# Kernel optimization log

Hardware: AMD Instinct MI355X
Metric: run time of the kernel (lower is better)

## Reference

```python
import jax, jax.numpy as jnp
import numpy as np

N = 30000      # nodes
E = 480000     # edges per relation (avg degree 16)
H = 4          # GAT heads
D = 64         # out_size per head
F1, F2 = 256, 128   # per-metapath input feature dims
SIN = 256      # sen_in_size
HD = H * D     # 256, semantic-attention in_size
OUT = 64       # final out_size


def _gat(feat, src, dst, W, al, ar, b):
    """DGL GATConv (eval mode, dropout=0), activation=relu6."""
    h = (feat @ W).reshape(N, H, D)                     # [N,H,D]
    el = (h * al).sum(-1)                               # [N,H]
    er = (h * ar).sum(-1)                               # [N,H]
    e = jax.nn.leaky_relu(el[src] + er[dst], 0.2)       # [E,H]
    m = jax.ops.segment_max(e, dst, N)                  # edge-softmax over incoming edges
    p = jnp.exp(e - m[dst])
    s = jax.ops.segment_sum(p, dst, N)
    a = p / s[dst]                                      # [E,H]
    out = jax.ops.segment_sum(a[:, :, None] * h[src], dst, N)  # [N,H,D]
    out = out + b.reshape(1, H, D)
    return jnp.clip(out, 0.0, 6.0).reshape(N, H * D)    # relu6, flatten(1)


def _gcn_layer(x, src, dst, W, b):
    """DGL GraphConv, norm='both': D_in^{-1/2} A D_out^{-1/2} X W (+ b)."""
    ones = jnp.ones(src.shape[0], x.dtype)
    deg_o = jnp.clip(jax.ops.segment_sum(ones, src, N), 1.0, None)
    deg_i = jnp.clip(jax.ops.segment_sum(ones, dst, N), 1.0, None)
    h = (x @ W) * (deg_o[:, None] ** -0.5)
    h = jax.ops.segment_sum(h[src], dst, N) * (deg_i[:, None] ** -0.5)
    return h if b is None else h + b


def setup_inputs():
    key = jax.random.key(0)
    ks = jax.random.split(key, 28)
    f32 = jnp.float32
    nrm = lambda k, shp: jax.random.normal(k, shp, f32) * 0.05
    ri = lambda k, shp: jax.random.randint(k, shp, 0, N, jnp.int32)
    return dict(
        feat0=jax.random.normal(ks[0], (N, F1), f32),
        feat1=jax.random.normal(ks[1], (N, F2), f32),
        sen_feat=jax.random.normal(ks[2], (N, SIN), f32),
        Wgat0=nrm(ks[11], (F1, H * D)), al0=nrm(ks[12], (H, D)), ar0=nrm(ks[13], (H, D)), b0=nrm(ks[14], (H * D,)),
        Wgat1=nrm(ks[15], (F2, H * D)), al1=nrm(ks[16], (H, D)), ar1=nrm(ks[17], (H, D)), b1=nrm(ks[18], (H * D,)),
        Wp1=nrm(ks[19], (HD, OUT)), bp1=nrm(ks[20], (OUT,)), wp2=nrm(ks[21], (OUT,)),
        Wf=nrm(ks[22], (HD, OUT)), bf=nrm(ks[23], (OUT,)),
        Wg1=nrm(ks[24], (SIN, OUT)), bg1=nrm(ks[25], (OUT,)), Wg2=nrm(ks[26], (OUT, OUT)),
        src0=ri(ks[3], (E,)), dst0=ri(ks[4], (E,)),
        src1=ri(ks[5], (E,)), dst1=ri(ks[6], (E,)),
        gsrc=ri(ks[7], (E,)), gdst=ri(ks[8], (E,)),
        asrc=ri(ks[9], (E,)), adst=ri(ks[10], (E,)),
        k=10,
    )


def reference(feat0, feat1, sen_feat,
              Wgat0, al0, ar0, b0, Wgat1, al1, ar1, b1,
              Wp1, bp1, wp2, Wf, bf, Wg1, bg1, Wg2,
              src0, dst0, src1, dst1, gsrc, gdst, asrc, adst, k):
    # per-metapath GAT embeddings
    z0 = _gat(feat0, src0, dst0, Wgat0, al0, ar0, b0)   # [N, HD]
    z1 = _gat(feat1, src1, dst1, Wgat1, al1, ar1, b1)   # [N, HD]
    z = jnp.stack([z0, z1], axis=1)                     # [N, M=2, HD]
    # PathAttention (semantic attention over metapaths)
    w = jnp.tanh(z @ Wp1 + bp1) @ wp2                   # [N, M]
    beta = jax.nn.softmax(w.mean(0))                    # [M]
    fused = jnp.einsum('m,nmf->nf', beta, z)            # [N, HD]
    Femb = fused @ Wf + bf                              # [N, OUT]
    # two-layer GCN on the sentence graph
    p1 = jnp.tanh(_gcn_layer(sen_feat, gsrc, gdst, Wg1, bg1))
    P = _gcn_layer(p1, gsrc, gdst, Wg2, None)           # [N, OUT]
    # spectral loss: fuse embeddings, trace of Laplacian quadratic form on first k dims
    Z = 0.5 * (Femb + P)                                # [N, OUT]
    Zk = Z[:, :k]
    diff = Zk[asrc] - Zk[adst]
    tr = 0.5 * jnp.sum(diff * diff)                     # tr(Zk^T (D - A) Zk)
    return (tr, Z)
```

## Files before the change

### kernel.cpp

```cpp
#include <hip/hip_runtime.h>
#include <math.h>

#define NN 30000
#define NE 480000
#define NBLK 118
#define NMT 235
#define NTRB 1875
#define CAPD 128

typedef unsigned short ushort_t;
typedef unsigned int uint_t;
typedef __attribute__((ext_vector_type(8))) short short8;
typedef __attribute__((ext_vector_type(4))) float f32x4;

__device__ __forceinline__ ushort_t f2bf(float x) {
  uint_t u = __float_as_uint(x);
  u = (u + 0x7FFF + ((u >> 16) & 1)) >> 16;
  return (ushort_t)u;
}
__device__ __forceinline__ float bf2f(ushort_t v) {
  return __uint_as_float(((uint_t)v) << 16);
}

__device__ __forceinline__ float wred(float v) {
#pragma unroll
  for (int off = 32; off > 0; off >>= 1) v += __shfl_xor(v, off);
  return v;
}

__global__ void prep_kernel(float4* __restrict__ zp, const float* __restrict__ W0,
                            const float* __restrict__ W1, const float* __restrict__ W2,
                            const float* __restrict__ W3, const float* __restrict__ W4,
                            ushort_t* __restrict__ T0, ushort_t* __restrict__ T1,
                            ushort_t* __restrict__ T2, ushort_t* __restrict__ T3,
                            ushort_t* __restrict__ T4) {
  int id = blockIdx.x * 256 + threadIdx.x;
  if (id < 52501) {
    zp[id] = make_float4(0.f, 0.f, 0.f, 0.f);
    return;
  }
  int wid = id - 52501;
  const float* W;
  ushort_t* T;
  int K, N, base;
  if (wid < 65536) { W = W0; T = T0; K = 256; N = 256; base = 0; }
  else if (wid < 98304) { W = W1; T = T1; K = 128; N = 256; base = 65536; }
  else if (wid < 114688) { W = W2; T = T2; K = 256; N = 64; base = 98304; }
  else if (wid < 131072) { W = W3; T = T3; K = 256; N = 64; base = 114688; }
  else if (wid < 147456) { W = W4; T = T4; K = 256; N = 64; base = 131072; }
  else return;
  int l = wid - base;
  int k = l / N, n = l - k * N;
  T[(size_t)n * K + k] = f2bf(W[l]);
}


__device__ __forceinline__ void mfma_core_f32(const float* __restrict__ A0,
                                              const ushort_t* __restrict__ BT, int K, int bm,
                                              short* __restrict__ As, short* __restrict__ Bs,
                                              f32x4 acc[2][4]) {
  int tid = threadIdx.x;
  int lane = tid & 63, w = tid >> 6;
  int q = lane >> 4, mr = lane & 15;
#pragma unroll 1
  for (int k0 = 0; k0 < K; k0 += 32) {
    {
      int r = tid >> 1, hf = tid & 1;
      int gr = bm + r;
      float4 f0 = make_float4(0.f, 0.f, 0.f, 0.f), f1 = f0, f2 = f0, f3 = f0;
      if (gr < NN) {
        const float4* pa = (const float4*)(A0 + (size_t)gr * K + k0 + hf * 16);
        f0 = pa[0]; f1 = pa[1]; f2 = pa[2]; f3 = pa[3];
      }
      short8 lo, hi;
      lo[0] = (short)f2bf(f0.x); lo[1] = (short)f2bf(f0.y);
      lo[2] = (short)f2bf(f0.z); lo[3] = (short)f2bf(f0.w);
      lo[4] = (short)f2bf(f1.x); lo[5] = (short)f2bf(f1.y);
      lo[6] = (short)f2bf(f1.z); lo[7] = (short)f2bf(f1.w);
      hi[0] = (short)f2bf(f2.x); hi[1] = (short)f2bf(f2.y);
      hi[2] = (short)f2bf(f2.z); hi[3] = (short)f2bf(f2.w);
      hi[4] = (short)f2bf(f3.x); hi[5] = (short)f2bf(f3.y);
      hi[6] = (short)f2bf(f3.z); hi[7] = (short)f2bf(f3.w);
      short* dst = As + r * 40 + hf * 16;
      *(short8*)(dst) = lo;
      *(short8*)(dst + 8) = hi;
    }
    {
      int n = tid >> 2, qk = tid & 3;
      short8 bv = *(const short8*)((const short*)BT + (size_t)n * K + k0 + qk * 8);
      *(short8*)(Bs + n * 40 + qk * 8) = bv;
    }
    __syncthreads();
    short8 a0 = *(short8*)(As + (w * 32 + mr) * 40 + q * 8);
    short8 a1 = *(short8*)(As + (w * 32 + 16 + mr) * 40 + q * 8);
#pragma unroll
    for (int j = 0; j < 4; ++j) {
      short8 b = *(short8*)(Bs + (j * 16 + mr) * 40 + q * 8);
      acc[0][j] = __builtin_amdgcn_mfma_f32_16x16x32_bf16(a0, b, acc[0][j], 0, 0, 0);
      acc[1][j] = __builtin_amdgcn_mfma_f32_16x16x32_bf16(a1, b, acc[1][j], 0, 0, 0);
    }
    __syncthreads();
  }
}

__device__ __forceinline__ void mfma_core2_f32(const float* __restrict__ A0,
                                               const ushort_t* __restrict__ BT, int K, int bm,
                                               short* __restrict__ As, short* __restrict__ Bs,
                                               f32x4 acc[2][8]) {
  int tid = threadIdx.x;
  int lane = tid & 63, w = tid >> 6;
  int q = lane >> 4, mr = lane & 15;
#pragma unroll 1
  for (int k0 = 0; k0 < K; k0 += 32) {
    {
      int r = tid >> 1, hf = tid & 1;
      int gr = bm + r;
      float4 f0 = make_float4(0.f, 0.f, 0.f, 0.f), f1 = f0, f2 = f0, f3 = f0;
      if (gr < NN) {
        const float4* pa = (const float4*)(A0 + (size_t)gr * K + k0 + hf * 16);
        f0 = pa[0]; f1 = pa[1]; f2 = pa[2]; f3 = pa[3];
      }
      short8 lo, hi;
      lo[0] = (short)f2bf(f0.x); lo[1] = (short)f2bf(f0.y);
      lo[2] = (short)f2bf(f0.z); lo[3] = (short)f2bf(f0.w);
      lo[4] = (short)f2bf(f1.x); lo[5] = (short)f2bf(f1.y);
      lo[6] = (short)f2bf(f1.z); lo[7] = (short)f2bf(f1.w);
      hi[0] = (short)f2bf(f2.x); hi[1] = (short)f2bf(f2.y);
      hi[2] = (short)f2bf(f2.z); hi[3] = (short)f2bf(f2.w);
      hi[4] = (short)f2bf(f3.x); hi[5] = (short)f2bf(f3.y);
      hi[6] = (short)f2bf(f3.z); hi[7] = (short)f2bf(f3.w);
      short* dst = As + r * 40 + hf * 16;
      *(short8*)(dst) = lo;
      *(short8*)(dst + 8) = hi;
    }
    {
      int n = tid >> 1, qk = tid & 1;
      const short* src = (const short*)BT + (size_t)n * K + k0 + qk * 16;
      short8 b0 = *(const short8*)src;
      short8 b1 = *(const short8*)(src + 8);
      short* d = Bs + n * 40 + qk * 16;
      *(short8*)d = b0;
      *(short8*)(d + 8) = b1;
    }
    __syncthreads();
    short8 a0 = *(short8*)(As + (w * 32 + mr) * 40 + q * 8);
    short8 a1 = *(short8*)(As + (w * 32 + 16 + mr) * 40 + q * 8);
#pragma unroll
    for (int j = 0; j < 8; ++j) {
      short8 b = *(short8*)(Bs + (j * 16 + mr) * 40 + q * 8);
      acc[0][j] = __builtin_amdgcn_mfma_f32_16x16x32_bf16(a0, b, acc[0][j], 0, 0, 0);
      acc[1][j] = __builtin_amdgcn_mfma_f32_16x16x32_bf16(a1, b, acc[1][j], 0, 0, 0);
    }
    __syncthreads();
  }
}

__device__ __forceinline__ void mfma_core2_bf(const ushort_t* __restrict__ A0,
                                              const ushort_t* __restrict__ BT, int bm,
                                              short* __restrict__ As, short* __restrict__ Bs,
                                              f32x4 acc[2][8]) {
  int tid = threadIdx.x;
  int lane = tid & 63, w = tid >> 6;
  int q = lane >> 4, mr = lane & 15;
#pragma unroll 1
  for (int k0 = 0; k0 < 256; k0 += 32) {
    {
      int r = tid >> 1, hf = tid & 1;
      int gr = bm + r;
      short8 v0 = {0, 0, 0, 0, 0, 0, 0, 0}, v1 = v0;
      if (gr < NN) {
        const short* p0 = (const short*)A0 + (size_t)gr * 256 + k0 + hf * 16;
        v0 = *(const short8*)p0;
        v1 = *(const short8*)(p0 + 8);
      }
      short* dst = As + r * 40 + hf * 16;
      *(short8*)(dst) = v0;
      *(short8*)(dst + 8) = v1;
    }
    {
      int n = tid >> 1, qk = tid & 1;
      const short* src = (const short*)BT + (size_t)n * 256 + k0 + qk * 16;
      short8 b0 = *(const short8*)src;
      short8 b1 = *(const short8*)(src + 8);
      short* d = Bs + n * 40 + qk * 16;
      *(short8*)d = b0;
      *(short8*)(d + 8) = b1;
    }
    __syncthreads();
    short8 a0 = *(short8*)(As + (w * 32 + mr) * 40 + q * 8);
    short8 a1 = *(short8*)(As + (w * 32 + 16 + mr) * 40 + q * 8);
#pragma unroll
    for (int j = 0; j < 8; ++j) {
      short8 b = *(short8*)(Bs + (j * 16 + mr) * 40 + q * 8);
      acc[0][j] = __builtin_amdgcn_mfma_f32_16x16x32_bf16(a0, b, acc[0][j], 0, 0, 0);
      acc[1][j] = __builtin_amdgcn_mfma_f32_16x16x32_bf16(a1, b, acc[1][j], 0, 0, 0);
    }
    __syncthreads();
  }
}

__global__ __launch_bounds__(256) void mfma_all_kernel(
    const float* __restrict__ feat0, const float* __restrict__ feat1,
    const float* __restrict__ sen, const ushort_t* __restrict__ WT0,
    const ushort_t* __restrict__ WT1, const ushort_t* __restrict__ Wg1T,
    ushort_t* __restrict__ h0, ushort_t* __restrict__ h1, ushort_t* __restrict__ gcnA,
    const float* __restrict__ al0, const float* __restrict__ ar0, float* __restrict__ el0,
    float* __restrict__ er0, const float* __restrict__ al1, const float* __restrict__ ar1,
    float* __restrict__ el1, float* __restrict__ er1, const float* __restrict__ rdo) {
  __shared__ short As[128 * 40];
  __shared__ short Bs[128 * 40];
  int y = blockIdx.y;
  int bm = blockIdx.x * 128;
  int lane = threadIdx.x & 63, w = threadIdx.x >> 6;
  int q = lane >> 4, mr = lane & 15;
  if (y < 4) {
    int gsel = y >> 1, p = y & 1;
    const float* A = gsel ? feat1 : feat0;
    int K = gsel ? 128 : 256;
    const ushort_t* WT = gsel ? WT1 : WT0;
    ushort_t* H = gsel ? h1 : h0;
    const float* al = gsel ? al1 : al0;
    const float* ar = gsel ? ar1 : ar0;
    float* el = gsel ? el1 : el0;
    float* er = gsel ? er1 : er0;
    f32x4 acc[2][8];
#pragma unroll
    for (int i = 0; i < 2; ++i)
#pragma unroll
      for (int j = 0; j < 8; ++j) acc[i][j] = (f32x4){0.f, 0.f, 0.f, 0.f};
    mfma_core2_f32(A, WT + (size_t)p * 128 * K, K, bm, As, Bs, acc);
    float alv[8], arv[8];
#pragma unroll
    for (int j = 0; j < 8; ++j) {
      alv[j] = al[p * 128 + j * 16 + mr];
      arv[j] = ar[p * 128 + j * 16 + mr];
    }
#pragma unroll
    for (int i = 0; i < 2; ++i)
#pragma unroll
      for (int r = 0; r < 4; ++r) {
        int gr = bm + w * 32 + i * 16 + q * 4 + r;
        float pl0 = 0.f, pr0 = 0.f, pl1 = 0.f, pr1 = 0.f;
#pragma unroll
        for (int j = 0; j < 4; ++j) {
          pl0 = fmaf(acc[i][j][r], alv[j], pl0);
          pr0 = fmaf(acc[i][j][r], arv[j], pr0);
          pl1 = fmaf(acc[i][j + 4][r], alv[j + 4], pl1);
          pr1 = fmaf(acc[i][j + 4][r], arv[j + 4], pr1);
        }
#pragma unroll
        for (int m = 1; m < 16; m <<= 1) {
          pl0 += __shfl_xor(pl0, m);
          pr0 += __shfl_xor(pr0, m);
          pl1 += __shfl_xor(pl1, m);
          pr1 += __shfl_xor(pr1, m);
        }
        if (gr < NN) {
          if (mr == 0) {
            el[gr * 4 + 2 * p] = pl0;
            er[gr * 4 + 2 * p] = pr0;
            el[gr * 4 + 2 * p + 1] = pl1;
            er[gr * 4 + 2 * p + 1] = pr1;
          }
#pragma unroll
          for (int j = 0; j < 8; ++j)
            H[(size_t)gr * 256 + p * 128 + j * 16 + mr] = f2bf(acc[i][j][r]);
        }
      }
  } else {
    f32x4 acc[2][4];
#pragma unroll
    for (int i = 0; i < 2; ++i)
#pragma unroll
      for (int j = 0; j < 4; ++j) acc[i][j] = (f32x4){0.f, 0.f, 0.f, 0.f};
    mfma_core_f32(sen, Wg1T, 256, bm, As, Bs, acc);
#pragma unroll
    for (int i = 0; i < 2; ++i)
#pragma unroll
      for (int r = 0; r < 4; ++r) {
        int gr = bm + w * 32 + i * 16 + q * 4 + r;
        if (gr < NN) {
          float sc = rdo[gr];
#pragma unroll
          for (int j = 0; j < 4; ++j)
            gcnA[(size_t)gr * 64 + j * 16 + mr] = f2bf(acc[i][j][r] * sc);
        }
      }
  }
}

__global__ __launch_bounds__(256) void mfma_attnwf_kernel(
    const ushort_t* __restrict__ z0, const ushort_t* __restrict__ z1,
    const ushort_t* __restrict__ WpfT, const float* __restrict__ bp1,
    const float* __restrict__ wp2, float* __restrict__ pbuf, ushort_t* __restrict__ Y0,
    ushort_t* __restrict__ Y1) {
  __shared__ short As[128 * 40];
  __shared__ short Bs[128 * 40];
  __shared__ float wsum[4];
  const ushort_t* A = blockIdx.y ? z1 : z0;
  ushort_t* Y = blockIdx.y ? Y1 : Y0;
  int bm = blockIdx.x * 128;
  f32x4 acc[2][8];
#pragma unroll
  for (int i = 0; i < 2; ++i)
#pragma unroll
    for (int j = 0; j < 8; ++j) acc[i][j] = (f32x4){0.f, 0.f, 0.f, 0.f};
  mfma_core2_bf(A, WpfT, bm, As, Bs, acc);
  int lane = threadIdx.x & 63, w = threadIdx.x >> 6;
  int q = lane >> 4, mr = lane & 15;
  float local = 0.f;
#pragma unroll
  for (int j = 0; j < 4; ++j) {
    int col = j * 16 + mr;
    float bp = bp1[col], wp = wp2[col];
#pragma unroll
    for (int i = 0; i < 2; ++i)
#pragma unroll
      for (int r = 0; r < 4; ++r) {
        int gr = bm + w * 32 + i * 16 + q * 4 + r;
        if (gr < NN) local += tanhf(acc[i][j][r] + bp) * wp;
      }
  }
  local = wred(local);
  if (lane == 0) wsum[w] = local;
#pragma unroll
  for (int j = 4; j < 8; ++j) {
    int col = (j - 4) * 16 + mr;
#pragma unroll
    for (int i = 0; i < 2; ++i)
#pragma unroll
      for (int r = 0; r < 4; ++r) {
        int gr = bm + w * 32 + i * 16 + q * 4 + r;
        if (gr < NN) Y[(size_t)gr * 64 + col] = f2bf(acc[i][j][r]);
      }
  }
  __syncthreads();
  if (threadIdx.x == 0)
    pbuf[blockIdx.y * NMT + blockIdx.x] = wsum[0] + wsum[1] + wsum[2] + wsum[3];
}

__global__ void hist_kernel(const int* __restrict__ d0, const int* __restrict__ d1,
                            const int* __restrict__ d2, const int* __restrict__ d3,
                            int* __restrict__ cnt) {
  int g = blockIdx.y;
  const int* d = g == 0 ? d0 : g == 1 ? d1 : g == 2 ? d2 : d3;
  int e = blockIdx.x * 256 + threadIdx.x;
  if (e < NE) atomicAdd(&cnt[g * NN + d[e]], 1);
}

__global__ __launch_bounds__(256) void scan_blocks_kernel(const int* __restrict__ cnt,
                                                          int* __restrict__ rows,
                                                          int* __restrict__ bsum) {
  __shared__ int sm[256];
  int g = blockIdx.y, t = threadIdx.x;
  int i = blockIdx.x * 256 + t;
  int v = (i < NN) ? cnt[g * NN + i] : 0;
  sm[t] = v;
  __syncthreads();
#pragma unroll
  for (int off = 1; off < 256; off <<= 1) {
    int tmp = (t >= off) ? sm[t - off] : 0;
    __syncthreads();
    sm[t] += tmp;
    __syncthreads();
  }
  if (i < NN) rows[g * (NN + 1) + i] = sm[t] - v;
  if (t == 255) bsum[g * NBLK + blockIdx.x] = sm[255];
}

__global__ __launch_bounds__(128) void scan_tops_kernel(int* __restrict__ bsum,
                                                        int* __restrict__ boff) {
  __shared__ int sm[128];
  int g = blockIdx.y, t = threadIdx.x;
  int v = (t < NBLK) ? bsum[g * NBLK + t] : 0;
  sm[t] = v;
  __syncthreads();
#pragma unroll
  for (int off = 1; off < 128; off <<= 1) {
    int tmp = (t >= off) ? sm[t - off] : 0;
    __syncthreads();
    sm[t] += tmp;
    __syncthreads();
  }
  if (t < NBLK) boff[g * NBLK + t] = sm[t] - v;
}

__global__ void add_off_kernel(int* __restrict__ rows, const int* __restrict__ boff) {
  int g = blockIdx.y, t = threadIdx.x;
  int i = blockIdx.x * 256 + t;
  if (i < NN) rows[g * (NN + 1) + i] += boff[g * NBLK + blockIdx.x];
  if (blockIdx.x == 0 && t == 0) rows[g * (NN + 1) + NN] = NE;
}

__global__ void scatter_kernel(const int* __restrict__ s0, const int* __restrict__ s1,
                               const int* __restrict__ s2, const int* __restrict__ d0,
                               const int* __restrict__ d1, const int* __restrict__ d2,
                               const int* __restrict__ rows, int* __restrict__ cnt2,
                               int* __restrict__ cols, const int* __restrict__ cnt_deg,
                               float* __restrict__ rdo, float* __restrict__ rdi,
                               const int* __restrict__ rows_g) {
  int g = blockIdx.y;
  if (g == 3) {
    int n = blockIdx.x * 256 + threadIdx.x;
    if (n < NN) {
      rdo[n] = rsqrtf(fmaxf((float)cnt_deg[n], 1.f));
      float di = (float)(rows_g[n + 1] - rows_g[n]);
      rdi[n] = rsqrtf(fmaxf(di, 1.f));
    }
    return;
  }
  const int* sp = g == 0 ? s0 : g == 1 ? s1 : s2;
  const int* dp = g == 0 ? d0 : g == 1 ? d1 : d2;
  int e = blockIdx.x * 256 + threadIdx.x;
  if (e >= NE) return;
  int d = dp[e];
  int pos = rows[g * (NN + 1) + d] + atomicAdd(&cnt2[g * NN + d], 1);
  cols[(size_t)g * NE + pos] = sp[e];
}

__global__ __launch_bounds__(256) void gat_node_kernel(
    const int* __restrict__ rows0, const int* __restrict__ cols0, const float* __restrict__ el0,
    const float* __restrict__ er0, const ushort_t* __restrict__ h0,
    const float* __restrict__ bias0, ushort_t* __restrict__ zz0, const int* __restrict__ rows1,
    const int* __restrict__ cols1, const float* __restrict__ el1, const float* __restrict__ er1,
    const ushort_t* __restrict__ h1, const float* __restrict__ bias1,
    ushort_t* __restrict__ zz1) {
  __shared__ float aw[4][CAPD][4];
  int g = blockIdx.y;
  const int* rows = g ? rows1 : rows0;
  const int* cols = g ? cols1 : cols0;
  const float* el = g ? el1 : el0;
  const float* er = g ? er1 : er0;
  const ushort_t* h = g ? h1 : h0;
  const float* bias = g ? bias1 : bias0;
  ushort_t* z = g ? zz1 : zz0;

  int lane = threadIdx.x & 63, w = threadIdx.x >> 6;
  int n = blockIdx.x * 4 + w;
  int r0 = rows[n], r1 = rows[n + 1];
  int deg = r1 - r0;
  float4 er4 = *(const float4*)&er[n * 4];
  float s0 = 0.f, s1 = 0.f, s2 = 0.f, s3 = 0.f;
  for (int j = lane; j < deg; j += 64) {
    int s = cols[r0 + j];
    float4 elv = *(const float4*)&el[s * 4];
    float v0 = elv.x + er4.x; v0 = v0 > 0.f ? v0 : 0.2f * v0;
    float v1 = elv.y + er4.y; v1 = v1 > 0.f ? v1 : 0.2f * v1;
    float v2 = elv.z + er4.z; v2 = v2 > 0.f ? v2 : 0.2f * v2;
    float v3 = elv.w + er4.w; v3 = v3 > 0.f ? v3 : 0.2f * v3;
    float e0 = __expf(v0), e1 = __expf(v1), e2 = __expf(v2), e3 = __expf(v3);
    s0 += e0; s1 += e1; s2 += e2; s3 += e3;
    if (j < CAPD) {
      aw[w][j][0] = e0; aw[w][j][1] = e1; aw[w][j][2] = e2; aw[w][j][3] = e3;
    }
  }
  s0 = wred(s0); s1 = wred(s1); s2 = wred(s2); s3 = wred(s3);
  __syncthreads();
  int hh = lane >> 4;
  float denom = hh == 0 ? s0 : hh == 1 ? s1 : hh == 2 ? s2 : s3;
  float myer = hh == 0 ? er4.x : hh == 1 ? er4.y : hh == 2 ? er4.z : er4.w;
  float invd = (deg > 0) ? 1.f / denom : 0.f;
  float4 acc = make_float4(0.f, 0.f, 0.f, 0.f);
  int jc = deg < CAPD ? deg : CAPD;
  int j = 0;
  for (; j + 8 <= jc; j += 8) {
    int si[8];
    float ai[8];
    ushort4 ui[8];
#pragma unroll
    for (int t = 0; t < 8; ++t) {
      si[t] = cols[r0 + j + t];
      ai[t] = aw[w][j + t][hh];
    }
#pragma unroll
    for (int t = 0; t < 8; ++t) ui[t] = *(const ushort4*)&h[(size_t)si[t] * 256 + lane * 4];
#pragma unroll
    for (int t = 0; t < 8; ++t) {
      acc.x = fmaf(ai[t], bf2f(ui[t].x), acc.x);
      acc.y = fmaf(ai[t], bf2f(ui[t].y), acc.y);
      acc.z = fmaf(ai[t], bf2f(ui[t].z), acc.z);
      acc.w = fmaf(ai[t], bf2f(ui[t].w), acc.w);
    }
  }
  for (; j + 4 <= jc; j += 4) {
    int sa = cols[r0 + j], sb = cols[r0 + j + 1], sc = cols[r0 + j + 2], sd = cols[r0 + j + 3];
    float aa = aw[w][j][hh], ab = aw[w][j + 1][hh], ac = aw[w][j + 2][hh], ad = aw[w][j + 3][hh];
    ushort4 ua = *(const ushort4*)&h[(size_t)sa * 256 + lane * 4];
    ushort4 ub = *(const ushort4*)&h[(size_t)sb * 256 + lane * 4];
    ushort4 uc = *(const ushort4*)&h[(size_t)sc * 256 + lane * 4];
    ushort4 ud = *(const ushort4*)&h[(size_t)sd * 256 + lane * 4];
    acc.x = fmaf(aa, bf2f(ua.x), acc.x); acc.y = fmaf(aa, bf2f(ua.y), acc.y);
    acc.z = fmaf(aa, bf2f(ua.z), acc.z); acc.w = fmaf(aa, bf2f(ua.w), acc.w);
    acc.x = fmaf(ab, bf2f(ub.x), acc.x); acc.y = fmaf(ab, bf2f(ub.y), acc.y);
    acc.z = fmaf(ab, bf2f(ub.z), acc.z); acc.w = fmaf(ab, bf2f(ub.w), acc.w);
    acc.x = fmaf(ac, bf2f(uc.x), acc.x); acc.y = fmaf(ac, bf2f(uc.y), acc.y);
    acc.z = fmaf(ac, bf2f(uc.z), acc.z); acc.w = fmaf(ac, bf2f(uc.w), acc.w);
    acc.x = fmaf(ad, bf2f(ud.x), acc.x); acc.y = fmaf(ad, bf2f(ud.y), acc.y);
    acc.z = fmaf(ad, bf2f(ud.z), acc.z); acc.w = fmaf(ad, bf2f(ud.w), acc.w);
  }
  for (; j < jc; ++j) {
    int s = cols[r0 + j];
    float a = aw[w][j][hh];
    ushort4 hu = *(const ushort4*)&h[(size_t)s * 256 + lane * 4];
    acc.x = fmaf(a, bf2f(hu.x), acc.x);
    acc.y = fmaf(a, bf2f(hu.y), acc.y);
    acc.z = fmaf(a, bf2f(hu.z), acc.z);
    acc.w = fmaf(a, bf2f(hu.w), acc.w);
  }
  for (; j < deg; ++j) {
    int s = cols[r0 + j];
    float v = el[s * 4 + hh] + myer;
    v = v > 0.f ? v : 0.2f * v;
    float a = __expf(v);
    ushort4 hu = *(const ushort4*)&h[(size_t)s * 256 + lane * 4];
    acc.x = fmaf(a, bf2f(hu.x), acc.x);
    acc.y = fmaf(a, bf2f(hu.y), acc.y);
    acc.z = fmaf(a, bf2f(hu.z), acc.z);
    acc.w = fmaf(a, bf2f(hu.w), acc.w);
  }
  float4 bv = *(const float4*)&bias[lane * 4];
  ushort4 o;
  o.x = f2bf(fminf(fmaxf(acc.x * invd + bv.x, 0.f), 6.f));
  o.y = f2bf(fminf(fmaxf(acc.y * invd + bv.y, 0.f), 6.f));
  o.z = f2bf(fminf(fmaxf(acc.z * invd + bv.z, 0.f), 6.f));
  o.w = f2bf(fminf(fmaxf(acc.w * invd + bv.w, 0.f), 6.f));
  *(ushort4*)&z[(size_t)n * 256 + lane * 4] = o;
}

__global__ __launch_bounds__(256) void gcn_gather12_kernel(
    const int* __restrict__ rows, const int* __restrict__ cols, const ushort_t* __restrict__ X,
    const float* __restrict__ rdi, const float* __restrict__ bg1, const float* __restrict__ Wg2,
    const float* __restrict__ rdo, ushort_t* __restrict__ out2, const float* __restrict__ pbuf,
    float* __restrict__ wb) {
  int lane = threadIdx.x & 63, w = threadIdx.x >> 6;
  if (blockIdx.x == 0) {
    __shared__ float sm[8];
    int t = threadIdx.x;
    float a0 = 0.f, a1 = 0.f;
    for (int i = t; i < NMT; i += 256) {
      a0 += pbuf[i];
      a1 += pbuf[NMT + i];
    }
    a0 = wred(a0);
    a1 = wred(a1);
    if (lane == 0) { sm[w] = a0; sm[4 + w] = a1; }
    __syncthreads();
    if (t == 0) {
      float w0 = (sm[0] + sm[1] + sm[2] + sm[3]) * (1.0f / NN);
      float w1 = (sm[4] + sm[5] + sm[6] + sm[7]) * (1.0f / NN);
      float mx = fmaxf(w0, w1);
      float e0 = expf(w0 - mx), e1 = expf(w1 - mx);
      float inv = 1.f / (e0 + e1);
      wb[2] = e0 * inv;
      wb[3] = e1 * inv;
    }
  }
  int n = blockIdx.x * 4 + w;
  if (n >= NN) return;
  int r0 = rows[n], r1 = rows[n + 1];
  float acc = 0.f;
  int j = r0;
  for (; j + 4 <= r1; j += 4) {
    int sa = cols[j], sb = cols[j + 1], sc = cols[j + 2], sd = cols[j + 3];
    acc += bf2f(X[(size_t)sa * 64 + lane]) + bf2f(X[(size_t)sb * 64 + lane]) +
           bf2f(X[(size_t)sc * 64 + lane]) + bf2f(X[(size_t)sd * 64 + lane]);
  }
  for (; j < r1; ++j) acc += bf2f(X[(size_t)cols[j] * 64 + lane]);
  float p = tanhf(acc * rdi[n] + bg1[lane]);
  float o = 0.f;
#pragma unroll
  for (int k = 0; k < 64; ++k) o = fmaf(__shfl(p, k), Wg2[k * 64 + lane], o);
  out2[(size_t)n * 64 + lane] = f2bf(o * rdo[n]);
}

__global__ __launch_bounds__(256) void gcn_gather2_kernel(
    const int* __restrict__ rows, const int* __restrict__ cols, const ushort_t* __restrict__ X,
    const float* __restrict__ rdi, const ushort_t* __restrict__ Y0,
    const ushort_t* __restrict__ Y1, const float* __restrict__ wb, const float* __restrict__ bf,
    const int* __restrict__ kptr, float* __restrict__ Zc, float* __restrict__ dout) {
  int lane = threadIdx.x & 63, w = threadIdx.x >> 6;
  int n = blockIdx.x * 4 + w;
  if (n >= NN) return;
  int r0 = rows[n], r1 = rows[n + 1];
  float acc = 0.f;
  int j = r0;
  for (; j + 4 <= r1; j += 4) {
    int sa = cols[j], sb = cols[j + 1], sc = cols[j + 2], sd = cols[j + 3];
    acc += bf2f(X[(size_t)sa * 64 + lane]) + bf2f(X[(size_t)sb * 64 + lane]) +
           bf2f(X[(size_t)sc * 64 + lane]) + bf2f(X[(size_t)sd * 64 + lane]);
  }
  for (; j < r1; ++j) acc += bf2f(X[(size_t)cols[j] * 64 + lane]);
  float femb = wb[2] * bf2f(Y0[(size_t)n * 64 + lane]) +
               wb[3] * bf2f(Y1[(size_t)n * 64 + lane]) + bf[lane];
  float zv = 0.5f * (femb + acc * rdi[n]);
  dout[1 + (size_t)n * 64 + lane] = zv;
  int k = *kptr;
  if (lane < k && lane < 16) Zc[(size_t)n * 16 + lane] = zv;
}

__global__ __launch_bounds__(256) void tr_kernel(const int* __restrict__ asrc,
                                                 const int* __restrict__ adst,
                                                 const int* __restrict__ kptr,
                                                 const float* __restrict__ Zc,
                                                 const float* __restrict__ dout,
                                                 float* __restrict__ trbuf) {
  __shared__ float wsum[4];
  int e = blockIdx.x * 256 + threadIdx.x;
  int k = *kptr;
  float local = 0.f;
  if (e < NE) {
    int a = asrc[e], b = adst[e];
    if (k <= 16) {
      const float* Za = Zc + (size_t)a * 16;
      const float* Zb = Zc + (size_t)b * 16;
      for (int c = 0; c < k; ++c) {
        float d2 = Za[c] - Zb[c];
        local += d2 * d2;
      }
    } else {
      const float* Za = dout + 1 + (size_t)a * 64;
      const float* Zb = dout + 1 + (size_t)b * 64;
      for (int c = 0; c < k; ++c) {
        float d2 = Za[c] - Zb[c];
        local += d2 * d2;
      }
    }
  }
#pragma unroll
  for (int off = 32; off > 0; off >>= 1) local += __shfl_down(local, off);
  int lane = threadIdx.x & 63, w = threadIdx.x >> 6;
  if (lane == 0) wsum[w] = local;
  __syncthreads();
  if (threadIdx.x == 0) trbuf[blockIdx.x] = wsum[0] + wsum[1] + wsum[2] + wsum[3];
}

__global__ __launch_bounds__(256) void tr_reduce_kernel(const float* __restrict__ trbuf,
                                                        float* __restrict__ dout) {
  __shared__ float sm[4];
  int t = threadIdx.x;
  float a = 0.f;
  for (int i = t; i < NTRB; i += 256) a += trbuf[i];
  a = wred(a);
  int lane = t & 63, w = t >> 6;
  if (lane == 0) sm[w] = a;
  __syncthreads();
  if (t == 0) dout[0] = 0.5f * (sm[0] + sm[1] + sm[2] + sm[3]);
}

extern "C" void kernel_launch(void* const* d_in, const int* in_sizes, int n_in, void* d_out,
                              int out_size, void* d_ws, size_t ws_size, hipStream_t stream) {
  const float* feat0 = (const float*)d_in[0];
  const float* feat1 = (const float*)d_in[1];
  const float* sen = (const float*)d_in[2];
  const float* Wgat0 = (const float*)d_in[3];
  const float* al0 = (const float*)d_in[4];
  const float* ar0 = (const float*)d_in[5];
  const float* b0 = (const float*)d_in[6];
  const float* Wgat1 = (const float*)d_in[7];
  const float* al1 = (const float*)d_in[8];
  const float* ar1 = (const float*)d_in[9];
  const float* b1 = (const float*)d_in[10];
  const float* Wp1 = (const float*)d_in[11];
  const float* bp1 = (const float*)d_in[12];
  const float* wp2 = (const float*)d_in[13];
  const float* Wf = (const float*)d_in[14];
  const float* bf = (const float*)d_in[15];
  const float* Wg1 = (const float*)d_in[16];
  const float* bg1 = (const float*)d_in[17];
  const float* Wg2 = (const float*)d_in[18];
  const int* src0 = (const int*)d_in[19];
  const int* dst0 = (const int*)d_in[20];
  const int* src1 = (const int*)d_in[21];
  const int* dst1 = (const int*)d_in[22];
  const int* gsrc = (const int*)d_in[23];
  const int* gdst = (const int*)d_in[24];
  const int* asrc = (const int*)d_in[25];
  const int* adst = (const int*)d_in[26];
  const int* kptr = (const int*)d_in[27];
  float* out = (float*)d_out;
  float* ws = (float*)d_ws;

  float* wb = ws;
  int* cnt = (int*)(ws + 4);
  int* cnt2 = (int*)(ws + 120004);
  float* rdo = ws + 210004;
  float* rdi = ws + 240004;
  int* rows = (int*)(ws + 270004);
  int* bsum = (int*)(ws + 360008);
  int* boff = (int*)(ws + 360364);
  int* cols = (int*)(ws + 360720);
  float* el0 = ws + 1800720;
  float* er0 = ws + 1920720;
  float* el1 = ws + 2040720;
  float* er1 = ws + 2160720;
  float* pbuf = ws + 2280720;
  float* trbuf = ws + 2281192;
  ushort_t* h0 = (ushort_t*)(ws + 2283068);
  ushort_t* h1 = (ushort_t*)(ws + 6123068);
  ushort_t* z0 = (ushort_t*)(ws + 9963068);
  ushort_t* z1 = (ushort_t*)(ws + 13803068);
  ushort_t* gcnA = (ushort_t*)(ws + 17643068);
  ushort_t* gcnA2 = (ushort_t*)(ws + 18603068);
  ushort_t* Y0 = (ushort_t*)(ws + 19563068);
  ushort_t* Y1 = (ushort_t*)(ws + 20523068);
  ushort_t* WT0 = (ushort_t*)(ws + 21483068);
  ushort_t* WT1 = (ushort_t*)(ws + 21515836);
  ushort_t* WpfT = (ushort_t*)(ws + 21532220);
  ushort_t* Wg1T = (ushort_t*)(ws + 21548604);
  float* Zc = ws + 21556796;

  int* rows_g = rows + 2 * (NN + 1);
  int* cols_g = cols + 2 * NE;
  int* cnt_deg = cnt + 3 * NN;

  prep_kernel<<<782, 256, 0, stream>>>((float4*)ws, Wgat0, Wgat1, Wp1, Wf, Wg1, WT0, WT1, WpfT,
                                       WpfT + 16384, Wg1T);

  hist_kernel<<<dim3(1875, 4), 256, 0, stream>>>(dst0, dst1, gdst, gsrc, cnt);
  scan_blocks_kernel<<<dim3(NBLK, 3), 256, 0, stream>>>(cnt, rows, bsum);
  scan_tops_kernel<<<dim3(1, 3), 128, 0, stream>>>(bsum, boff);
  add_off_kernel<<<dim3(NBLK, 3), 256, 0, stream>>>(rows, boff);
  scatter_kernel<<<dim3(1875, 4), 256, 0, stream>>>(src0, src1, gsrc, dst0, dst1, gdst, rows,
                                                    cnt2, cols, cnt_deg, rdo, rdi, rows_g);

  mfma_all_kernel<<<dim3(NMT, 5), 256, 0, stream>>>(feat0, feat1, sen, WT0, WT1, Wg1T, h0, h1,
                                                    gcnA, al0, ar0, el0, er0, al1, ar1, el1,
                                                    er1, rdo);

  gat_node_kernel<<<dim3(7500, 2), 256, 0, stream>>>(rows, cols, el0, er0, h0, b0, z0,
                                                     rows + (NN + 1), cols + NE, el1, er1, h1,
                                                     b1, z1);

  mfma_attnwf_kernel<<<dim3(NMT, 2), 256, 0, stream>>>(z0, z1, WpfT, bp1, wp2, pbuf, Y0, Y1);

  gcn_gather12_kernel<<<7500, 256, 0, stream>>>(rows_g, cols_g, gcnA, rdi, bg1, Wg2, rdo, gcnA2,
                                                pbuf, wb);
  gcn_gather2_kernel<<<7500, 256, 0, stream>>>(rows_g, cols_g, gcnA2, rdi, Y0, Y1, wb, bf, kptr,
                                               Zc, out);

  tr_kernel<<<NTRB, 256, 0, stream>>>(asrc, adst, kptr, Zc, out, trbuf);
  tr_reduce_kernel<<<1, 256, 0, stream>>>(trbuf, out);
}
```

Before: 549.9 us.

## Widen gather loads by splitting wave lanes across several edges per step

The GAT aggregation now has each half-wave handle alternate edges, loading 16-byte bf16 vectors per lane, and combines the two halves with a cross-lane shuffle. The GCN gathers likewise give each 16-lane group its own edge with 8-byte loads, reduce the groups with shuffles, and pass the sums through shared memory. The trace kernel assigns 4 lanes per edge with float4 loads of the compacted Zk, which means more blocks and a larger partial-sum buffer that now reuses the el0 workspace. The aim is fewer, wider memory instructions and more independent gathers in flight, at the cost of extra shuffle reductions, more registers and some idle lanes on odd-degree tails.

```diff
diff --git a/kernel.cpp b/kernel.cpp
--- a/kernel.cpp
+++ b/kernel.cpp
@@ -5,7 +5,7 @@
 #define NE 480000
 #define NBLK 118
 #define NMT 235
-#define NTRB 1875
+#define NTRB 7500
 #define CAPD 128
 
 typedef unsigned short ushort_t;
@@ -456,75 +456,71 @@
   }
   s0 = wred(s0); s1 = wred(s1); s2 = wred(s2); s3 = wred(s3);
   __syncthreads();
-  int hh = lane >> 4;
+  int par = lane >> 5;
+  int fl = lane & 31;
+  int hh = fl >> 3;
   float denom = hh == 0 ? s0 : hh == 1 ? s1 : hh == 2 ? s2 : s3;
   float myer = hh == 0 ? er4.x : hh == 1 ? er4.y : hh == 2 ? er4.z : er4.w;
   float invd = (deg > 0) ? 1.f / denom : 0.f;
-  float4 acc = make_float4(0.f, 0.f, 0.f, 0.f);
+  float facc[8];
+#pragma unroll
+  for (int u = 0; u < 8; ++u) facc[u] = 0.f;
   int jc = deg < CAPD ? deg : CAPD;
   int j = 0;
-  for (; j + 8 <= jc; j += 8) {
+  for (; j + 16 <= jc; j += 16) {
     int si[8];
     float ai[8];
-    ushort4 ui[8];
 #pragma unroll
     for (int t = 0; t < 8; ++t) {
-      si[t] = cols[r0 + j + t];
-      ai[t] = aw[w][j + t][hh];
-    }
-#pragma unroll
-    for (int t = 0; t < 8; ++t) ui[t] = *(const ushort4*)&h[(size_t)si[t] * 256 + lane * 4];
-#pragma unroll
-    for (int t = 0; t < 8; ++t) {
-      acc.x = fmaf(ai[t], bf2f(ui[t].x), acc.x);
-      acc.y = fmaf(ai[t], bf2f(ui[t].y), acc.y);
-      acc.z = fmaf(ai[t], bf2f(ui[t].z), acc.z);
-      acc.w = fmaf(ai[t], bf2f(ui[t].w), acc.w);
-    }
-  }
-  for (; j + 4 <= jc; j += 4) {
-    int sa = cols[r0 + j], sb = cols[r0 + j + 1], sc = cols[r0 + j + 2], sd = cols[r0 + j + 3];
-    float aa = aw[w][j][hh], ab = aw[w][j + 1][hh], ac = aw[w][j + 2][hh], ad = aw[w][j + 3][hh];
-    ushort4 ua = *(const ushort4*)&h[(size_t)sa * 256 + lane * 4];
-    ushort4 ub = *(const ushort4*)&h[(size_t)sb * 256 + lane * 4];
-    ushort4 uc = *(const ushort4*)&h[(size_t)sc * 256 + lane * 4];
-    ushort4 ud = *(const ushort4*)&h[(size_t)sd * 256 + lane * 4];
-    acc.x = fmaf(aa, bf2f(ua.x), acc.x); acc.y = fmaf(aa, bf2f(ua.y), acc.y);
-    acc.z = fmaf(aa, bf2f(ua.z), acc.z); acc.w = fmaf(aa, bf2f(ua.w), acc.w);
-    acc.x = fmaf(ab, bf2f(ub.x), acc.x); acc.y = fmaf(ab, bf2f(ub.y), acc.y);
-    acc.z = fmaf(ab, bf2f(ub.z), acc.z); acc.w = fmaf(ab, bf2f(ub.w), acc.w);
-    acc.x = fmaf(ac, bf2f(uc.x), acc.x); acc.y = fmaf(ac, bf2f(uc.y), acc.y);
-    acc.z = fmaf(ac, bf2f(uc.z), acc.z); acc.w = fmaf(ac, bf2f(uc.w), acc.w);
-    acc.x = fmaf(ad, bf2f(ud.x), acc.x); acc.y = fmaf(ad, bf2f(ud.y), acc.y);
-    acc.z = fmaf(ad, bf2f(ud.z), acc.z); acc.w = fmaf(ad, bf2f(ud.w), acc.w);
-  }
-  for (; j < jc; ++j) {
+      si[t] = cols[r0 + j + 2 * t + par];
+      ai[t] = aw[w][j + 2 * t + par][hh];
+    }
+    short8 hv[8];
+#pragma unroll
+    for (int t = 0; t < 8; ++t) hv[t] = *(const short8*)&h[(size_t)si[t] * 256 + fl * 8];
+#pragma unroll
+    for (int t = 0; t < 8; ++t)
+#pragma unroll
+      for (int u = 0; u < 8; ++u) facc[u] = fmaf(ai[t], bf2f((ushort_t)hv[t][u]), facc[u]);
+  }
+  for (; j + 2 <= jc; j += 2) {
+    int s = cols[r0 + j + par];
+    float a = aw[w][j + par][hh];
+    short8 hv = *(const short8*)&h[(size_t)s * 256 + fl * 8];
+#pragma unroll
+    for (int u = 0; u < 8; ++u) facc[u] = fmaf(a, bf2f((ushort_t)hv[u]), facc[u]);
+  }
+  if (j < jc) {
     int s = cols[r0 + j];
-    float a = aw[w][j][hh];
-    ushort4 hu = *(const ushort4*)&h[(size_t)s * 256 + lane * 4];
-    acc.x = fmaf(a, bf2f(hu.x), acc.x);
-    acc.y = fmaf(a, bf2f(hu.y), acc.y);
-    acc.z = fmaf(a, bf2f(hu.z), acc.z);
-    acc.w = fmaf(a, bf2f(hu.w), acc.w);
+    float a = par ? 0.f : aw[w][j][hh];
+    short8 hv = *(const short8*)&h[(size_t)s * 256 + fl * 8];
+#pragma unroll
+    for (int u = 0; u < 8; ++u) facc[u] = fmaf(a, bf2f((ushort_t)hv[u]), facc[u]);
+    j = jc;
   }
   for (; j < deg; ++j) {
     int s = cols[r0 + j];
     float v = el[s * 4 + hh] + myer;
     v = v > 0.f ? v : 0.2f * v;
-    float a = __expf(v);
-    ushort4 hu = *(const ushort4*)&h[(size_t)s * 256 + lane * 4];
-    acc.x = fmaf(a, bf2f(hu.x), acc.x);
-    acc.y = fmaf(a, bf2f(hu.y), acc.y);
-    acc.z = fmaf(a, bf2f(hu.z), acc.z);
-    acc.w = fmaf(a, bf2f(hu.w), acc.w);
-  }
-  float4 bv = *(const float4*)&bias[lane * 4];
-  ushort4 o;
-  o.x = f2bf(fminf(fmaxf(acc.x * invd + bv.x, 0.f), 6.f));
-  o.y = f2bf(fminf(fmaxf(acc.y * invd + bv.y, 0.f), 6.f));
-  o.z = f2bf(fminf(fmaxf(acc.z * invd + bv.z, 0.f), 6.f));
-  o.w = f2bf(fminf(fmaxf(acc.w * invd + bv.w, 0.f), 6.f));
-  *(ushort4*)&z[(size_t)n * 256 + lane * 4] = o;
+    float a = par ? 0.f : __expf(v);
+    short8 hv = *(const short8*)&h[(size_t)s * 256 + fl * 8];
+#pragma unroll
+    for (int u = 0; u < 8; ++u) facc[u] = fmaf(a, bf2f((ushort_t)hv[u]), facc[u]);
+  }
+#pragma unroll
+  for (int u = 0; u < 8; ++u) facc[u] += __shfl_xor(facc[u], 32);
+  if (par == 0) {
+    float4 bv0 = *(const float4*)&bias[fl * 8];
+    float4 bv1 = *(const float4*)&bias[fl * 8 + 4];
+    float bb[8] = {bv0.x, bv0.y, bv0.z, bv0.w, bv1.x, bv1.y, bv1.z, bv1.w};
+    short8 o;
+#pragma unroll
+    for (int u = 0; u < 8; ++u) {
+      float v = fminf(fmaxf(facc[u] * invd + bb[u], 0.f), 6.f);
+      o[u] = (short)f2bf(v);
+    }
+    *(short8*)&z[(size_t)n * 256 + fl * 8] = o;
+  }
 }
 
 __global__ __launch_bounds__(256) void gcn_gather12_kernel(
@@ -532,6 +528,7 @@
     const float* __restrict__ rdi, const float* __restrict__ bg1, const float* __restrict__ Wg2,
     const float* __restrict__ rdo, ushort_t* __restrict__ out2, const float* __restrict__ pbuf,
     float* __restrict__ wb) {
+  __shared__ float psm[4][64];
   int lane = threadIdx.x & 63, w = threadIdx.x >> 6;
   if (blockIdx.x == 0) {
     __shared__ float sm[8];
@@ -558,15 +555,49 @@
   int n = blockIdx.x * 4 + w;
   if (n >= NN) return;
   int r0 = rows[n], r1 = rows[n + 1];
-  float acc = 0.f;
+  int eg = lane >> 4, fl = lane & 15;
+  float facc[4] = {0.f, 0.f, 0.f, 0.f};
   int j = r0;
+  for (; j + 16 <= r1; j += 16) {
+    int si[4];
+#pragma unroll
+    for (int t = 0; t < 4; ++t) si[t] = cols[j + 4 * t + eg];
+    ushort4 xv[4];
+#pragma unroll
+    for (int t = 0; t < 4; ++t) xv[t] = *(const ushort4*)&X[(size_t)si[t] * 64 + fl * 4];
+#pragma unroll
+    for (int t = 0; t < 4; ++t) {
+      facc[0] += bf2f(xv[t].x);
+      facc[1] += bf2f(xv[t].y);
+      facc[2] += bf2f(xv[t].z);
+      facc[3] += bf2f(xv[t].w);
+    }
+  }
   for (; j + 4 <= r1; j += 4) {
-    int sa = cols[j], sb = cols[j + 1], sc = cols[j + 2], sd = cols[j + 3];
-    acc += bf2f(X[(size_t)sa * 64 + lane]) + bf2f(X[(size_t)sb * 64 + lane]) +
-           bf2f(X[(size_t)sc * 64 + lane]) + bf2f(X[(size_t)sd * 64 + lane]);
-  }
-  for (; j < r1; ++j) acc += bf2f(X[(size_t)cols[j] * 64 + lane]);
-  float p = tanhf(acc * rdi[n] + bg1[lane]);
+    int s = cols[j + eg];
+    ushort4 xv = *(const ushort4*)&X[(size_t)s * 64 + fl * 4];
+    facc[0] += bf2f(xv.x);
+    facc[1] += bf2f(xv.y);
+    facc[2] += bf2f(xv.z);
+    facc[3] += bf2f(xv.w);
+  }
+  int rem = r1 - j;
+  if (eg < rem) {
+    int s = cols[j + eg];
+    ushort4 xv = *(const ushort4*)&X[(size_t)s * 64 + fl * 4];
+    facc[0] += bf2f(xv.x);
+    facc[1] += bf2f(xv.y);
+    facc[2] += bf2f(xv.z);
+    facc[3] += bf2f(xv.w);
+  }
+#pragma unroll
+  for (int u = 0; u < 4; ++u) {
+    facc[u] += __shfl_xor(facc[u], 16);
+    facc[u] += __shfl_xor(facc[u], 32);
+  }
+  if (eg == 0) *(float4*)&psm[w][fl * 4] = make_float4(facc[0], facc[1], facc[2], facc[3]);
+  __syncthreads();
+  float p = tanhf(psm[w][lane] * rdi[n] + bg1[lane]);
   float o = 0.f;
 #pragma unroll
   for (int k = 0; k < 64; ++k) o = fmaf(__shfl(p, k), Wg2[k * 64 + lane], o);
@@ -582,20 +613,69 @@
   int n = blockIdx.x * 4 + w;
   if (n >= NN) return;
   int r0 = rows[n], r1 = rows[n + 1];
-  float acc = 0.f;
+  int eg = lane >> 4, fl = lane & 15;
+  float facc[4] = {0.f, 0.f, 0.f, 0.f};
   int j = r0;
+  for (; j + 16 <= r1; j += 16) {
+    int si[4];
+#pragma unroll
+    for (int t = 0; t < 4; ++t) si[t] = cols[j + 4 * t + eg];
+    ushort4 xv[4];
+#pragma unroll
+    for (int t = 0; t < 4; ++t) xv[t] = *(const ushort4*)&X[(size_t)si[t] * 64 + fl * 4];
+#pragma unroll
+    for (int t = 0; t < 4; ++t) {
+      facc[0] += bf2f(xv[t].x);
+      facc[1] += bf2f(xv[t].y);
+      facc[2] += bf2f(xv[t].z);
+      facc[3] += bf2f(xv[t].w);
+    }
+  }
   for (; j + 4 <= r1; j += 4) {
-    int sa = cols[j], sb = cols[j + 1], sc = cols[j + 2], sd = cols[j + 3];
-    acc += bf2f(X[(size_t)sa * 64 + lane]) + bf2f(X[(size_t)sb * 64 + lane]) +
-           bf2f(X[(size_t)sc * 64 + lane]) + bf2f(X[(size_t)sd * 64 + lane]);
-  }
-  for (; j < r1; ++j) acc += bf2f(X[(size_t)cols[j] * 64 + lane]);
-  float femb = wb[2] * bf2f(Y0[(size_t)n * 64 + lane]) +
-               wb[3] * bf2f(Y1[(size_t)n * 64 + lane]) + bf[lane];
-  float zv = 0.5f * (femb + acc * rdi[n]);
-  dout[1 + (size_t)n * 64 + lane] = zv;
-  int k = *kptr;
-  if (lane < k && lane < 16) Zc[(size_t)n * 16 + lane] = zv;
+    int s = cols[j + eg];
+    ushort4 xv = *(const ushort4*)&X[(size_t)s * 64 + fl * 4];
+    facc[0] += bf2f(xv.x);
+    facc[1] += bf2f(xv.y);
+    facc[2] += bf2f(xv.z);
+    facc[3] += bf2f(xv.w);
+  }
+  int rem = r1 - j;
+  if (eg < rem) {
+    int s = cols[j + eg];
+    ushort4 xv = *(const ushort4*)&X[(size_t)s * 64 + fl * 4];
+    facc[0] += bf2f(xv.x);
+    facc[1] += bf2f(xv.y);
+    facc[2] += bf2f(xv.z);
+    facc[3] += bf2f(xv.w);
+  }
+#pragma unroll
+  for (int u = 0; u < 4; ++u) {
+    facc[u] += __shfl_xor(facc[u], 16);
+    facc[u] += __shfl_xor(facc[u], 32);
+  }
+  if (eg == 0) {
+    float ri = rdi[n];
+    ushort4 y0 = *(const ushort4*)&Y0[(size_t)n * 64 + fl * 4];
+    ushort4 y1 = *(const ushort4*)&Y1[(size_t)n * 64 + fl * 4];
+    float4 bfv = *(const float4*)&bf[fl * 4];
+    float w2 = wb[2], w3 = wb[3];
+    float zv[4];
+    zv[0] = 0.5f * (w2 * bf2f(y0.x) + w3 * bf2f(y1.x) + bfv.x + facc[0] * ri);
+    zv[1] = 0.5f * (w2 * bf2f(y0.y) + w3 * bf2f(y1.y) + bfv.y + facc[1] * ri);
+    zv[2] = 0.5f * (w2 * bf2f(y0.z) + w3 * bf2f(y1.z) + bfv.z + facc[2] * ri);
+    zv[3] = 0.5f * (w2 * bf2f(y0.w) + w3 * bf2f(y1.w) + bfv.w + facc[3] * ri);
+    float* dp = dout + 1 + (size_t)n * 64 + fl * 4;
+    dp[0] = zv[0]; dp[1] = zv[1]; dp[2] = zv[2]; dp[3] = zv[3];
+    int k = *kptr;
+    if (fl < 4) {
+      float4 zk;
+      zk.x = (fl * 4 + 0 < k) ? zv[0] : 0.f;
+      zk.y = (fl * 4 + 1 < k) ? zv[1] : 0.f;
+      zk.z = (fl * 4 + 2 < k) ? zv[2] : 0.f;
+      zk.w = (fl * 4 + 3 < k) ? zv[3] : 0.f;
+      *(float4*)&Zc[(size_t)n * 16 + fl * 4] = zk;
+    }
+  }
 }
 
 __global__ __launch_bounds__(256) void tr_kernel(const int* __restrict__ asrc,
@@ -605,30 +685,36 @@
                                                  const float* __restrict__ dout,
                                                  float* __restrict__ trbuf) {
   __shared__ float wsum[4];
-  int e = blockIdx.x * 256 + threadIdx.x;
+  int lane = threadIdx.x & 63, w = threadIdx.x >> 6;
   int k = *kptr;
+  int eg = lane >> 2, c0 = (lane & 3) * 4;
+  int e = blockIdx.x * 64 + w * 16 + eg;
   float local = 0.f;
   if (e < NE) {
     int a = asrc[e], b = adst[e];
     if (k <= 16) {
-      const float* Za = Zc + (size_t)a * 16;
-      const float* Zb = Zc + (size_t)b * 16;
-      for (int c = 0; c < k; ++c) {
-        float d2 = Za[c] - Zb[c];
-        local += d2 * d2;
-      }
+      float4 za = *(const float4*)&Zc[(size_t)a * 16 + c0];
+      float4 zb = *(const float4*)&Zc[(size_t)b * 16 + c0];
+      float dx = za.x - zb.x, dy = za.y - zb.y, dz = za.z - zb.z, dw = za.w - zb.w;
+      local = dx * dx + dy * dy + dz * dz + dw * dw;
     } else {
       const float* Za = dout + 1 + (size_t)a * 64;
       const float* Zb = dout + 1 + (size_t)b * 64;
-      for (int c = 0; c < k; ++c) {
-        float d2 = Za[c] - Zb[c];
-        local += d2 * d2;
+#pragma unroll
+      for (int st = 0; st < 4; ++st) {
+#pragma unroll
+        for (int t = 0; t < 4; ++t) {
+          int c = c0 + st * 16 + t;
+          if (c < k) {
+            float d2 = Za[c] - Zb[c];
+            local += d2 * d2;
+          }
+        }
       }
     }
   }
 #pragma unroll
   for (int off = 32; off > 0; off >>= 1) local += __shfl_down(local, off);
-  int lane = threadIdx.x & 63, w = threadIdx.x >> 6;
   if (lane == 0) wsum[w] = local;
   __syncthreads();
   if (threadIdx.x == 0) trbuf[blockIdx.x] = wsum[0] + wsum[1] + wsum[2] + wsum[3];
@@ -694,7 +780,7 @@
   float* el1 = ws + 2040720;
   float* er1 = ws + 2160720;
   float* pbuf = ws + 2280720;
-  float* trbuf = ws + 2281192;
+  float* trbuf = el0;
   ushort_t* h0 = (ushort_t*)(ws + 2283068);
   ushort_t* h1 = (ushort_t*)(ws + 6123068);
   ushort_t* z0 = (ushort_t*)(ws + 9963068);
```

Measured after the change: 543.3 us. Within noise of the previous version (-1.2%).
